# Performance work log

Measured on AMD Instinct MI355X. Metric: run time of the kernel, lower is better.

Reference implementation:

```python
import jax, jax.numpy as jnp
import numpy as np

TAU = 2.0
BN_EPS = 1e-5
SG_ALPHA = 4.0
ATTN_SCALE = 0.125
NUM_HEADS = 8
T, B, C, H, W = 2, 16, 256, 64, 64


@jax.custom_vjp
def heaviside(x):
    return (x >= 0.0).astype(x.dtype)

def _hv_fwd(x):
    return (x >= 0.0).astype(x.dtype), x

def _hv_bwd(x, g):
    s = jax.nn.sigmoid(SG_ALPHA * x)
    return (g * SG_ALPHA * s * (1.0 - s),)

heaviside.defvjp(_hv_fwd, _hv_bwd)


def lif(x_seq, v_th):
    # MultiStepLIFNode: v <- v + (x - v)/tau ; spike = H(v - v_th); hard reset to 0 (detached)
    def step(v, x):
        v = v + (x - v) / TAU
        s = heaviside(v - v_th)
        v = v * (1.0 - jax.lax.stop_gradient(s))
        return v, s
    _, spikes = jax.lax.scan(step, jnp.zeros_like(x_seq[0]), x_seq)
    return spikes


def bn1d(x, gamma, beta, mean, var):
    # eval-mode BatchNorm1d over channel axis 2 of [T,B,C,N]
    inv = (gamma / jnp.sqrt(var + BN_EPS)).reshape(1, 1, -1, 1)
    shift = (beta - mean * gamma / jnp.sqrt(var + BN_EPS)).reshape(1, 1, -1, 1)
    return x * inv + shift


def to_heads(t):
    # [T,B,C,N] -> [T,B,h,N,d]
    t_, b_, c_, n_ = t.shape
    d = c_ // NUM_HEADS
    return t.transpose(0, 1, 3, 2).reshape(t_, b_, n_, NUM_HEADS, d).transpose(0, 1, 3, 2, 4)


def setup_inputs() -> dict:
    key = jax.random.key(0)
    ks = jax.random.split(key, 24)
    w_scale = 0.06  # ~1/sqrt(C)
    inp = {
        'x': jax.random.normal(ks[0], (T, B, C, H, W), jnp.float32),
        'wq': jax.random.normal(ks[1], (C, C), jnp.float32) * w_scale,
        'wk': jax.random.normal(ks[2], (C, C), jnp.float32) * w_scale,
        'wv': jax.random.normal(ks[3], (C, C), jnp.float32) * w_scale,
        'wp': jax.random.normal(ks[4], (C, C), jnp.float32) * w_scale,
        'bp': jax.random.normal(ks[5], (C,), jnp.float32) * 0.1,
    }
    i = 6
    for p in ('q', 'k', 'v', 'p'):
        inp[p + '_gamma'] = jax.random.uniform(ks[i], (C,), jnp.float32, 0.5, 1.5); i += 1
        inp[p + '_beta'] = jax.random.normal(ks[i], (C,), jnp.float32) * 0.1; i += 1
        inp[p + '_mean'] = jax.random.normal(ks[i], (C,), jnp.float32) * 0.1; i += 1
        inp[p + '_var'] = jax.random.uniform(ks[i], (C,), jnp.float32, 0.5, 1.5); i += 1
    return inp


def reference(x, wq, wk, wv, wp, bp,
              q_gamma, q_beta, q_mean, q_var,
              k_gamma, k_beta, k_mean, k_var,
              v_gamma, v_beta, v_mean, v_var,
              p_gamma, p_beta, p_mean, p_var):
    t_, b_, c_, h_, w_ = x.shape
    n_ = h_ * w_
    xs = lif(x, 1.0).reshape(t_, b_, c_, n_)  # proj_lif then flatten(3)
    # 1x1 conv == channel matmul, then BN, then LIF (binary spikes)
    q_out = lif(bn1d(jnp.einsum('oc,tbcn->tbon', wq, xs), q_gamma, q_beta, q_mean, q_var), 1.0)
    k_out = lif(bn1d(jnp.einsum('oc,tbcn->tbon', wk, xs), k_gamma, k_beta, k_mean, k_var), 1.0)
    v_out = lif(bn1d(jnp.einsum('oc,tbcn->tbon', wv, xs), v_gamma, v_beta, v_mean, v_var), 1.0)
    q = to_heads(q_out)
    k = to_heads(k_out)
    v = to_heads(v_out)
    # linear attention: (k^T @ v) then q @ (k^T v)
    kv = jnp.einsum('tbhnd,tbhne->tbhde', k, v)  # [T,B,h,d,d]
    attn = jnp.einsum('tbhnd,tbhde->tbhne', q, kv) * ATTN_SCALE
    attn = attn.transpose(0, 1, 2, 4, 3).reshape(t_, b_, c_, n_)
    s = lif(attn, 0.5)  # attn_lif with v_threshold=0.5
    out = jnp.einsum('oc,tbcn->tbon', wp, s) + bp.reshape(1, 1, -1, 1)
    out = bn1d(out, p_gamma, p_beta, p_mean, p_var).reshape(t_, b_, c_, h_, w_)
    return (out, xs, q_out, k_out, v_out)
```

## Files before the change

kernel.cpp:

```cpp
#include <hip/hip_runtime.h>
#include <cstdint>
#include <cstddef>

typedef __attribute__((ext_vector_type(8))) short short8;
typedef __attribute__((ext_vector_type(4))) float floatx4;
typedef __attribute__((ext_vector_type(4))) unsigned int uintx4;
typedef __attribute__((ext_vector_type(4))) unsigned short ushort4x;

#define DEV static __device__ __forceinline__

constexpr int NT = 2, NB = 16, NC = 256, NN = 4096, NHD = 8;
constexpr size_t NE1 = (size_t)NT * NB * NC * NN;
constexpr size_t TSTRIDE = (size_t)NB * NC * NN;

DEV unsigned short f2bf(float x) {
  unsigned int u = __builtin_bit_cast(unsigned int, x);
  unsigned int lsb = (u >> 16) & 1u;
  u += 0x7FFFu + lsb;
  return (unsigned short)(u >> 16);
}
DEV float bfb2f(unsigned short h) {
  unsigned int u = ((unsigned int)h) << 16;
  return __builtin_bit_cast(float, u);
}
DEV unsigned short spike2bf(float s) {
  return (unsigned short)(__builtin_bit_cast(unsigned int, s) >> 16);
}
DEV unsigned int pk2(unsigned short a, unsigned short b) {
  return (unsigned int)a | ((unsigned int)b << 16);
}
DEV int swz(int fr, int kk) { return fr * 4 + (kk ^ ((fr >> 1) & 3)); }
typedef __attribute__((address_space(3))) unsigned int lds_u32;
typedef __attribute__((address_space(1))) const unsigned int glb_u32;
DEV void gld_lds16(const void* g, void* l) {
  __builtin_amdgcn_global_load_lds((glb_u32*)g, (lds_u32*)l, 16, 0, 0);
}

__global__ __launch_bounds__(256) void prep_kernel(
    const float* __restrict__ wq, const float* __restrict__ wk, const float* __restrict__ wv,
    const float* __restrict__ wp, const float* __restrict__ bp,
    const float* __restrict__ qg, const float* __restrict__ qb, const float* __restrict__ qm, const float* __restrict__ qva,
    const float* __restrict__ kg, const float* __restrict__ kb, const float* __restrict__ km, const float* __restrict__ kva,
    const float* __restrict__ vg, const float* __restrict__ vb, const float* __restrict__ vm, const float* __restrict__ vva,
    const float* __restrict__ pg, const float* __restrict__ pb, const float* __restrict__ pm, const float* __restrict__ pva,
    unsigned short* __restrict__ Wqkv, unsigned short* __restrict__ Wp,
    float* __restrict__ invqkv, float* __restrict__ shqkv,
    float* __restrict__ invp, float* __restrict__ shp)
{
  int idx = blockIdx.x * 256 + threadIdx.x;
  if (idx < 196608) {
    int o = idx >> 8, c = idx & 255;
    const float* src = (o < 256) ? wq : (o < 512) ? wk : wv;
    float w = src[(size_t)(o & 255) * 256 + c];
    unsigned short h0 = f2bf(w);  float f0 = bfb2f(h0);
    float r1 = w - f0;
    unsigned short h1 = f2bf(r1); float f1 = bfb2f(h1);
    float r2 = r1 - f1;
    unsigned short h2 = f2bf(r2);
    Wqkv[idx] = h0; Wqkv[196608 + idx] = h1; Wqkv[393216 + idx] = h2;
  } else if (idx < 262144) {
    int j = idx - 196608;
    float w = wp[j];
    unsigned short h0 = f2bf(w);  float f0 = bfb2f(h0);
    float r1 = w - f0;
    unsigned short h1 = f2bf(r1); float f1 = bfb2f(h1);
    float r2 = r1 - f1;
    unsigned short h2 = f2bf(r2);
    Wp[j] = h0; Wp[65536 + j] = h1; Wp[131072 + j] = h2;
  } else if (idx < 262912) {
    int i = idx - 262144;
    int p = i >> 8, c = i & 255;
    float g  = (p == 0) ? qg[c] : (p == 1) ? kg[c] : vg[c];
    float be = (p == 0) ? qb[c] : (p == 1) ? kb[c] : vb[c];
    float mn = (p == 0) ? qm[c] : (p == 1) ? km[c] : vm[c];
    float vr = (p == 0) ? qva[c] : (p == 1) ? kva[c] : vva[c];
    float sq = sqrtf(vr + 1e-5f);
    invqkv[i] = g / sq;
    shqkv[i]  = be - (mn * g) / sq;
  } else if (idx < 263168) {
    int c = idx - 262912;
    float sq = sqrtf(pva[c] + 1e-5f);
    float iv = pg[c] / sq;
    invp[c] = iv;
    shp[c]  = pb[c] - (pm[c] * pg[c]) / sq + bp[c] * iv;
  }
}

__global__ __launch_bounds__(256) void lifx_kernel(const float* __restrict__ x,
                                                   float* __restrict__ xs_out,
                                                   unsigned short* __restrict__ xs_t)
{
  __shared__ float tile[2][64][65];
  const int nt = blockIdx.x, ct = blockIdx.y, b = blockIdx.z;
  const int tid = threadIdx.x;
  const int ci = tid >> 2, cq = tid & 3;
  const int n0 = nt * 64, c0 = ct * 64;
  const size_t rowbase = ((size_t)(b * NC + c0 + ci)) * NN + n0 + cq * 16;
  const float* px0 = x + rowbase;
  const float* px1 = x + rowbase + TSTRIDE;
  float* po0 = xs_out + rowbase;
  float* po1 = xs_out + rowbase + TSTRIDE;
  #pragma unroll
  for (int jj = 0; jj < 4; jj++) {
    floatx4 x0 = *(const floatx4*)(px0 + jj * 4);
    floatx4 x1 = *(const floatx4*)(px1 + jj * 4);
    floatx4 s0v, s1v;
    #pragma unroll
    for (int e = 0; e < 4; e++) {
      float v1 = x0[e] * 0.5f;
      float s0 = (v1 >= 1.0f) ? 1.0f : 0.0f;
      float vr = v1 * (1.0f - s0);
      float v2 = vr + (x1[e] - vr) * 0.5f;
      float s1 = (v2 >= 1.0f) ? 1.0f : 0.0f;
      s0v[e] = s0; s1v[e] = s1;
      tile[0][ci][cq * 16 + jj * 4 + e] = s0;
      tile[1][ci][cq * 16 + jj * 4 + e] = s1;
    }
    *(floatx4*)(po0 + jj * 4) = s0v;
    *(floatx4*)(po1 + jj * 4) = s1v;
  }
  __syncthreads();
  const int ni = tid >> 2, cg = tid & 3;
  #pragma unroll
  for (int t = 0; t < 2; t++) {
    unsigned short* dst = xs_t + ((size_t)((t * NB + b) * NN) + n0 + ni) * NC + c0 + cg * 16;
    uintx4 w0, w1;
    #pragma unroll
    for (int p2 = 0; p2 < 4; p2++) {
      w0[p2] = pk2(spike2bf(tile[t][cg * 16 + p2 * 2    ][ni]),
                   spike2bf(tile[t][cg * 16 + p2 * 2 + 1][ni]));
      w1[p2] = pk2(spike2bf(tile[t][cg * 16 + p2 * 2 + 8][ni]),
                   spike2bf(tile[t][cg * 16 + p2 * 2 + 9][ni]));
    }
    *(uintx4*)dst = w0;
    *(uintx4*)(dst + 8) = w1;
  }
}

__global__ __launch_bounds__(256, 3) void qkv_gemm(
    const unsigned short* __restrict__ xs_t,
    const unsigned short* __restrict__ Wsp,
    const float* __restrict__ invv, const float* __restrict__ shv,
    float* __restrict__ dq, float* __restrict__ dk, float* __restrict__ dv,
    unsigned short* __restrict__ qbits, unsigned short* __restrict__ kbits,
    unsigned short* __restrict__ vbits)
{
  __shared__ __align__(16) unsigned char smem[33280];
  unsigned short* Al = (unsigned short*)smem;
  unsigned short* Bl = (unsigned short*)(smem + 24576);
  float* yl = (float*)smem;
  const int nt = blockIdx.x, mt = blockIdx.y, b = blockIdx.z;
  const int tid = threadIdx.x;
  const int lane = tid & 63, quad = lane >> 4, l16 = lane & 15;
  const int wave = tid >> 6;
  const int tw = wave >> 1, wm = (wave & 1) * 64;
  floatx4 acc[4][4] = {};

  for (int k0 = 0; k0 < 256; k0 += 32) {
    __syncthreads();
    #pragma unroll
    for (int j = 0; j < 6; j++) {
      int ci = j * 256 + tid;
      int fr = ci >> 2;
      int kk = (ci & 3) ^ ((fr >> 1) & 3);
      int s = fr >> 7, row = fr & 127;
      const unsigned short* g = Wsp + (size_t)s * 196608 + (size_t)(mt * 128 + row) * 256 + k0 + kk * 8;
      gld_lds16(g, Al + (size_t)ci * 8);
    }
    #pragma unroll
    for (int j = 0; j < 2; j++) {
      int ci = j * 256 + tid;
      int fr = ci >> 2;
      int kk = (ci & 3) ^ ((fr >> 1) & 3);
      int t = fr >> 6, row = fr & 63;
      const unsigned short* g = xs_t + ((size_t)((t * NB + b) * NN) + nt * 64 + row) * NC + k0 + kk * 8;
      gld_lds16(g, Bl + (size_t)ci * 8);
    }
    __syncthreads();

    short8 bfr[4];
    #pragma unroll
    for (int ni = 0; ni < 4; ni++) {
      int fr = tw * 64 + ni * 16 + l16;
      bfr[ni] = *(const short8*)(Bl + (size_t)swz(fr, quad) * 8);
    }
    #pragma unroll
    for (int mi = 0; mi < 4; mi++) {
      const int r0 = wm + mi * 16 + l16;
      short8 a0 = *(const short8*)(Al + (size_t)swz(      r0, quad) * 8);
      short8 a1 = *(const short8*)(Al + (size_t)swz(128 + r0, quad) * 8);
      short8 a2 = *(const short8*)(Al + (size_t)swz(256 + r0, quad) * 8);
      #pragma unroll
      for (int ni = 0; ni < 4; ni++) {
        acc[mi][ni] = __builtin_amdgcn_mfma_f32_16x16x32_bf16(a0, bfr[ni], acc[mi][ni], 0, 0, 0);
        acc[mi][ni] = __builtin_amdgcn_mfma_f32_16x16x32_bf16(a1, bfr[ni], acc[mi][ni], 0, 0, 0);
        acc[mi][ni] = __builtin_amdgcn_mfma_f32_16x16x32_bf16(a2, bfr[ni], acc[mi][ni], 0, 0, 0);
      }
    }
  }
  __syncthreads();
  if (tw == 0) {
    #pragma unroll
    for (int mi = 0; mi < 4; mi++)
      #pragma unroll
      for (int r = 0; r < 4; r++)
        #pragma unroll
        for (int ni = 0; ni < 4; ni++)
          yl[(size_t)(wm + mi * 16 + quad * 4 + r) * 65 + ni * 16 + l16] = acc[mi][ni][r];
  }
  __syncthreads();
  if (tw == 1) {
    #pragma unroll
    for (int mi = 0; mi < 4; mi++) {
      #pragma unroll
      for (int r = 0; r < 4; r++) {
        const int lrow = wm + mi * 16 + quad * 4 + r;
        const int orow = mt * 128 + lrow;
        const float iv = invv[orow], sh = shv[orow];
        const int widx = orow >> 8, c = orow & 255;
        float* dst = (widx == 0) ? dq : (widx == 1) ? dk : dv;
        unsigned short* bb = (widx == 0) ? qbits : (widx == 1) ? kbits : vbits;
        #pragma unroll
        for (int ni = 0; ni < 4; ni++) {
          const int n = nt * 64 + ni * 16 + l16;
          float y0 = yl[(size_t)lrow * 65 + ni * 16 + l16] * iv + sh;
          float y1 = acc[mi][ni][r] * iv + sh;
          float v1 = y0 * 0.5f;
          float s0 = (v1 >= 1.0f) ? 1.0f : 0.0f;
          float vr = v1 * (1.0f - s0);
          float v2 = vr + (y1 - vr) * 0.5f;
          float s1 = (v2 >= 1.0f) ? 1.0f : 0.0f;
          dst[(size_t)(b * NC + c) * NN + n] = s0;
          dst[(size_t)((NB + b) * NC + c) * NN + n] = s1;
          unsigned long long bl0 = __ballot(s0 != 0.0f);
          unsigned long long bl1 = __ballot(s1 != 0.0f);
          if (l16 == 0) {
            const int w16 = nt * 4 + ni;
            bb[(size_t)b        * 65536 + (size_t)c * 256 + w16] = (unsigned short)(bl0 >> (quad * 16));
            bb[(size_t)(NB + b) * 65536 + (size_t)c * 256 + w16] = (unsigned short)(bl1 >> (quad * 16));
          }
        }
      }
    }
  }
}

__global__ __launch_bounds__(256) void kv_kernel(const unsigned long long* __restrict__ kb,
                                                 const unsigned long long* __restrict__ vb,
                                                 float* __restrict__ kvout)
{
  __shared__ unsigned long long Kl[32 * 65];
  __shared__ unsigned long long Vl[32 * 65];
  const int h = blockIdx.x, z = blockIdx.y;
  const int tid = threadIdx.x;
  for (int i = tid; i < 2048; i += 256) {
    int row = i >> 6, w = i & 63;
    size_t g = (size_t)z * 16384 + (size_t)(h * 32 + row) * 64 + w;
    Kl[row * 65 + w] = kb[g];
    Vl[row * 65 + w] = vb[g];
  }
  __syncthreads();
  const int d = tid & 31, e0 = tid >> 5;
  int acc0 = 0, acc1 = 0, acc2 = 0, acc3 = 0;
  for (int w = 0; w < 64; w++) {
    unsigned long long ku = Kl[d * 65 + w];
    acc0 += __popcll(ku & Vl[(e0     ) * 65 + w]);
    acc1 += __popcll(ku & Vl[(e0 +  8) * 65 + w]);
    acc2 += __popcll(ku & Vl[(e0 + 16) * 65 + w]);
    acc3 += __popcll(ku & Vl[(e0 + 24) * 65 + w]);
  }
  float* o = kvout + ((size_t)(z * NHD + h) << 10);
  o[d * 32 + e0     ] = (float)acc0;
  o[d * 32 + e0 +  8] = (float)acc1;
  o[d * 32 + e0 + 16] = (float)acc2;
  o[d * 32 + e0 + 24] = (float)acc3;
}

__global__ __launch_bounds__(256) void attn_kernel(const unsigned short* __restrict__ qb16,
                                                   const float* __restrict__ kvout,
                                                   unsigned short* __restrict__ sb16)
{
  __shared__ float kvl[2][32][33];
  __shared__ unsigned short qt[2][32][16];
  const int nb = blockIdx.x, h = blockIdx.y, b = blockIdx.z;
  const int tid = threadIdx.x;
  const int wave = tid >> 6, lane = tid & 63, quad = lane >> 4, l16 = lane & 15;
  for (int i = tid; i < 2048; i += 256) {
    int t = i >> 10, j = i & 1023;
    kvl[t][j >> 5][j & 31] = kvout[((size_t)((t * NB + b) * NHD + h) << 10) + j];
  }
  for (int i = tid; i < 1024; i += 256) {
    int t = i >> 9, j = i & 511, row = j >> 4, w = j & 15;
    qt[t][row][w] = qb16[(size_t)(t * NB + b) * 65536 + (size_t)(h * 32 + row) * 256 + nb * 16 + w];
  }
  __syncthreads();
  short8 bf[2][2][2];
  #pragma unroll
  for (int t = 0; t < 2; t++) {
    #pragma unroll
    for (int eh = 0; eh < 2; eh++) {
      short8 bh, bl;
      #pragma unroll
      for (int j = 0; j < 8; j++) {
        float v = kvl[t][quad * 8 + j][eh * 16 + l16];
        unsigned short h0 = f2bf(v);
        float lo = v - bfb2f(h0);
        bh[j] = (short)h0;
        bl[j] = (short)f2bf(lo);
      }
      bf[t][0][eh] = bh; bf[t][1][eh] = bl;
    }
  }
  floatx4 acc[2][4][2] = {};
  #pragma unroll
  for (int t = 0; t < 2; t++) {
    #pragma unroll
    for (int nt = 0; nt < 4; nt++) {
      const int wv = wave * 4 + nt;
      short8 af;
      #pragma unroll
      for (int j = 0; j < 8; j++) {
        unsigned short w = qt[t][quad * 8 + j][wv];
        af[j] = (short)(((w >> l16) & 1) ? 0x3F80 : 0);
      }
      #pragma unroll
      for (int eh = 0; eh < 2; eh++) {
        acc[t][nt][eh] = __builtin_amdgcn_mfma_f32_16x16x32_bf16(af, bf[t][0][eh], acc[t][nt][eh], 0, 0, 0);
        acc[t][nt][eh] = __builtin_amdgcn_mfma_f32_16x16x32_bf16(af, bf[t][1][eh], acc[t][nt][eh], 0, 0, 0);
      }
    }
  }
  const int n0 = nb * 256 + wave * 64;
  #pragma unroll
  for (int nt = 0; nt < 4; nt++) {
    #pragma unroll
    for (int r = 0; r < 4; r++) {
      const int n = n0 + nt * 16 + quad * 4 + r;
      #pragma unroll
      for (int eh = 0; eh < 2; eh++) {
        float a0 = acc[0][nt][eh][r] * 0.125f;
        float a1 = acc[1][nt][eh][r] * 0.125f;
        float v1 = a0 * 0.5f;
        float s0 = (v1 >= 0.5f) ? 1.f : 0.f;
        float vr = v1 * (1.f - s0);
        float v2 = vr + (a1 - vr) * 0.5f;
        float s1 = (v2 >= 0.5f) ? 1.f : 0.f;
        unsigned long long bl0 = __ballot(s0 != 0.f);
        unsigned long long bl1 = __ballot(s1 != 0.f);
        if (l16 == 0) {
          const int w16 = h * 2 + eh;
          sb16[(size_t)b        * 65536 + (size_t)n * 16 + w16] = (unsigned short)(bl0 >> (quad * 16));
          sb16[(size_t)(NB + b) * 65536 + (size_t)n * 16 + w16] = (unsigned short)(bl1 >> (quad * 16));
        }
      }
    }
  }
}

__global__ __launch_bounds__(256, 3) void p_gemm(
    const unsigned short* __restrict__ sb16,
    const unsigned short* __restrict__ Wsp,
    const float* __restrict__ invv, const float* __restrict__ shv,
    float* __restrict__ dout)
{
  __shared__ __align__(16) unsigned char smem[32768];
  unsigned short* Al = (unsigned short*)smem;
  unsigned short* Bl = (unsigned short*)(smem + 24576);
  const int nt = blockIdx.x, mt = blockIdx.y, z = blockIdx.z;
  const int tid = threadIdx.x;
  const int lane = tid & 63, quad = lane >> 4, l16 = lane & 15;
  const int wave = tid >> 6;
  const int wm = (wave & 1) * 64, wn = (wave >> 1) * 64;
  floatx4 acc[4][4] = {};
  const int brow = tid & 127, bhalf = tid >> 7;

  for (int k0 = 0; k0 < 256; k0 += 32) {
    __syncthreads();
    #pragma unroll
    for (int j = 0; j < 6; j++) {
      int ci = j * 256 + tid;
      int fr = ci >> 2;
      int kk = (ci & 3) ^ ((fr >> 1) & 3);
      int s = fr >> 7, row = fr & 127;
      const unsigned short* g = Wsp + (size_t)s * 65536 + (size_t)(mt * 128 + row) * 256 + k0 + kk * 8;
      gld_lds16(g, Al + (size_t)ci * 8);
    }
    {
      unsigned short wb = sb16[(size_t)z * 65536 + (size_t)(nt * 128 + brow) * 16 + (k0 >> 4) + bhalf];
      uintx4 lo4, hi4;
      #pragma unroll
      for (int p = 0; p < 4; p++) {
        lo4[p] = pk2(((wb >> (2 * p)) & 1) ? 0x3F80 : 0, ((wb >> (2 * p + 1)) & 1) ? 0x3F80 : 0);
        hi4[p] = pk2(((wb >> (8 + 2 * p)) & 1) ? 0x3F80 : 0, ((wb >> (9 + 2 * p)) & 1) ? 0x3F80 : 0);
      }
      *(uintx4*)(Bl + (size_t)swz(brow, bhalf * 2)     * 8) = lo4;
      *(uintx4*)(Bl + (size_t)swz(brow, bhalf * 2 + 1) * 8) = hi4;
    }
    __syncthreads();

    short8 bfr[4];
    #pragma unroll
    for (int ni = 0; ni < 4; ni++) {
      int fr = wn + ni * 16 + l16;
      bfr[ni] = *(const short8*)(Bl + (size_t)swz(fr, quad) * 8);
    }
    #pragma unroll
    for (int mi = 0; mi < 4; mi++) {
      const int r0 = wm + mi * 16 + l16;
      short8 a0 = *(const short8*)(Al + (size_t)swz(      r0, quad) * 8);
      short8 a1 = *(const short8*)(Al + (size_t)swz(128 + r0, quad) * 8);
      short8 a2 = *(const short8*)(Al + (size_t)swz(256 + r0, quad) * 8);
      #pragma unroll
      for (int ni = 0; ni < 4; ni++) {
        acc[mi][ni] = __builtin_amdgcn_mfma_f32_16x16x32_bf16(a0, bfr[ni], acc[mi][ni], 0, 0, 0);
        acc[mi][ni] = __builtin_amdgcn_mfma_f32_16x16x32_bf16(a1, bfr[ni], acc[mi][ni], 0, 0, 0);
        acc[mi][ni] = __builtin_amdgcn_mfma_f32_16x16x32_bf16(a2, bfr[ni], acc[mi][ni], 0, 0, 0);
      }
    }
  }
  #pragma unroll
  for (int mi = 0; mi < 4; mi++) {
    #pragma unroll
    for (int r = 0; r < 4; r++) {
      const int orow = mt * 128 + wm + mi * 16 + quad * 4 + r;
      const float iv = invv[orow], sh = shv[orow];
      #pragma unroll
      for (int ni = 0; ni < 4; ni++) {
        const int n = nt * 128 + wn + ni * 16 + l16;
        dout[((size_t)(z * NC + orow)) * NN + n] = acc[mi][ni][r] * iv + sh;
      }
    }
  }
}

extern "C" void kernel_launch(void* const* d_in, const int* in_sizes, int n_in,
                              void* d_out, int out_size, void* d_ws, size_t ws_size,
                              hipStream_t stream) {
  (void)in_sizes; (void)n_in; (void)out_size; (void)ws_size;
  const float* x  = (const float*)d_in[0];
  const float* wq = (const float*)d_in[1];
  const float* wk = (const float*)d_in[2];
  const float* wv = (const float*)d_in[3];
  const float* wp = (const float*)d_in[4];
  const float* bp = (const float*)d_in[5];
  const float* qg = (const float*)d_in[6],  *qb = (const float*)d_in[7];
  const float* qm = (const float*)d_in[8],  *qva = (const float*)d_in[9];
  const float* kg = (const float*)d_in[10], *kb = (const float*)d_in[11];
  const float* km = (const float*)d_in[12], *kva = (const float*)d_in[13];
  const float* vg = (const float*)d_in[14], *vb = (const float*)d_in[15];
  const float* vm = (const float*)d_in[16], *vva = (const float*)d_in[17];
  const float* pg = (const float*)d_in[18], *pb = (const float*)d_in[19];
  const float* pm = (const float*)d_in[20], *pva = (const float*)d_in[21];

  float* out = (float*)d_out;
  float* xs  = out + NE1;
  float* dq  = out + 2 * NE1;
  float* dk  = out + 3 * NE1;
  float* dv  = out + 4 * NE1;

  char* ws = (char*)d_ws;
  unsigned short* xs_t  = (unsigned short*)ws;
  unsigned short* Wqkv  = (unsigned short*)(ws + 67108864);
  unsigned short* Wp    = (unsigned short*)(ws + 68288512);
  float* kvout          = (float*)(ws + 68681728);
  unsigned short* qbits = (unsigned short*)(ws + 69730304);
  unsigned short* kbits = (unsigned short*)(ws + 73924608);
  unsigned short* vbits = (unsigned short*)(ws + 78118912);
  unsigned short* sbits = (unsigned short*)(ws + 82313216);
  float* invqkv         = (float*)(ws + 86507520);
  float* shqkv          = invqkv + 768;
  float* invp           = shqkv + 768;
  float* shp            = invp + 256;

  prep_kernel<<<1028, 256, 0, stream>>>(wq, wk, wv, wp, bp,
                                        qg, qb, qm, qva, kg, kb, km, kva,
                                        vg, vb, vm, vva, pg, pb, pm, pva,
                                        Wqkv, Wp, invqkv, shqkv, invp, shp);
  lifx_kernel<<<dim3(64, 4, 16), 256, 0, stream>>>(x, xs, xs_t);
  qkv_gemm<<<dim3(64, 6, 16), 256, 0, stream>>>(xs_t, Wqkv, invqkv, shqkv,
                                                dq, dk, dv, qbits, kbits, vbits);
  kv_kernel<<<dim3(8, 32), 256, 0, stream>>>((const unsigned long long*)kbits,
                                             (const unsigned long long*)vbits, kvout);
  attn_kernel<<<dim3(16, 8, 16), 256, 0, stream>>>(qbits, kvout, sbits);
  p_gemm<<<dim3(32, 2, 32), 256, 0, stream>>>(sbits, Wp, invp, shp, out);
}
```

Before: 1.035 ms.

## Store input spikes as packed bitmasks and expand to bf16 in GEMM

The LIF input kernel now writes the spike tensor as 16-bit bitmasks per 16 channels instead of a transposed bf16 copy, shrinking that intermediate sixteen-fold. The QKV GEMM reads the bitmask words and expands them into bf16 ones and zeros in registers before writing the swizzled LDS tile, replacing the async global-to-LDS loads for the B operand. This cuts global write and read traffic for the intermediate. It adds ALU work and synchronous LDS stores inside the GEMM loop, and issues small 2-byte global loads.

```diff
diff --git a/kernel.cpp b/kernel.cpp
--- a/kernel.cpp
+++ b/kernel.cpp
@@ -5,7 +5,6 @@
 typedef __attribute__((ext_vector_type(8))) short short8;
 typedef __attribute__((ext_vector_type(4))) float floatx4;
 typedef __attribute__((ext_vector_type(4))) unsigned int uintx4;
-typedef __attribute__((ext_vector_type(4))) unsigned short ushort4x;
 
 #define DEV static __device__ __forceinline__
 
@@ -22,9 +21,6 @@
 DEV float bfb2f(unsigned short h) {
   unsigned int u = ((unsigned int)h) << 16;
   return __builtin_bit_cast(float, u);
-}
-DEV unsigned short spike2bf(float s) {
-  return (unsigned short)(__builtin_bit_cast(unsigned int, s) >> 16);
 }
 DEV unsigned int pk2(unsigned short a, unsigned short b) {
   return (unsigned int)a | ((unsigned int)b << 16);
@@ -88,7 +84,7 @@
 
 __global__ __launch_bounds__(256) void lifx_kernel(const float* __restrict__ x,
                                                    float* __restrict__ xs_out,
-                                                   unsigned short* __restrict__ xs_t)
+                                                   unsigned short* __restrict__ xb16)
 {
   __shared__ float tile[2][64][65];
   const int nt = blockIdx.x, ct = blockIdx.y, b = blockIdx.z;
@@ -123,22 +119,16 @@
   const int ni = tid >> 2, cg = tid & 3;
   #pragma unroll
   for (int t = 0; t < 2; t++) {
-    unsigned short* dst = xs_t + ((size_t)((t * NB + b) * NN) + n0 + ni) * NC + c0 + cg * 16;
-    uintx4 w0, w1;
-    #pragma unroll
-    for (int p2 = 0; p2 < 4; p2++) {
-      w0[p2] = pk2(spike2bf(tile[t][cg * 16 + p2 * 2    ][ni]),
-                   spike2bf(tile[t][cg * 16 + p2 * 2 + 1][ni]));
-      w1[p2] = pk2(spike2bf(tile[t][cg * 16 + p2 * 2 + 8][ni]),
-                   spike2bf(tile[t][cg * 16 + p2 * 2 + 9][ni]));
-    }
-    *(uintx4*)dst = w0;
-    *(uintx4*)(dst + 8) = w1;
+    unsigned int wbits = 0;
+    #pragma unroll
+    for (int j = 0; j < 16; j++)
+      wbits |= (tile[t][cg * 16 + j][ni] != 0.f ? 1u : 0u) << j;
+    xb16[((size_t)((t * NB + b) * NN) + n0 + ni) * 16 + (c0 >> 4) + cg] = (unsigned short)wbits;
   }
 }
 
 __global__ __launch_bounds__(256, 3) void qkv_gemm(
-    const unsigned short* __restrict__ xs_t,
+    const unsigned short* __restrict__ xb16,
     const unsigned short* __restrict__ Wsp,
     const float* __restrict__ invv, const float* __restrict__ shv,
     float* __restrict__ dq, float* __restrict__ dk, float* __restrict__ dv,
@@ -155,6 +145,8 @@
   const int wave = tid >> 6;
   const int tw = wave >> 1, wm = (wave & 1) * 64;
   floatx4 acc[4][4] = {};
+  const int bt = tid >> 7, brow = (tid >> 1) & 63, bhalf = tid & 1;
+  const unsigned short* xrow = xb16 + ((size_t)((bt * NB + b) * NN) + nt * 64 + brow) * 16 + bhalf;
 
   for (int k0 = 0; k0 < 256; k0 += 32) {
     __syncthreads();
@@ -167,14 +159,17 @@
       const unsigned short* g = Wsp + (size_t)s * 196608 + (size_t)(mt * 128 + row) * 256 + k0 + kk * 8;
       gld_lds16(g, Al + (size_t)ci * 8);
     }
-    #pragma unroll
-    for (int j = 0; j < 2; j++) {
-      int ci = j * 256 + tid;
-      int fr = ci >> 2;
-      int kk = (ci & 3) ^ ((fr >> 1) & 3);
-      int t = fr >> 6, row = fr & 63;
-      const unsigned short* g = xs_t + ((size_t)((t * NB + b) * NN) + nt * 64 + row) * NC + k0 + kk * 8;
-      gld_lds16(g, Bl + (size_t)ci * 8);
+    {
+      unsigned int wb = xrow[k0 >> 4];
+      uintx4 c0v, c1v;
+      #pragma unroll
+      for (int p = 0; p < 4; p++) {
+        c0v[p] = pk2(((wb >> (2 * p)) & 1) ? 0x3F80 : 0, ((wb >> (2 * p + 1)) & 1) ? 0x3F80 : 0);
+        c1v[p] = pk2(((wb >> (8 + 2 * p)) & 1) ? 0x3F80 : 0, ((wb >> (9 + 2 * p)) & 1) ? 0x3F80 : 0);
+      }
+      int fr = bt * 64 + brow;
+      *(uintx4*)(Bl + (size_t)swz(fr, bhalf * 2)     * 8) = c0v;
+      *(uintx4*)(Bl + (size_t)swz(fr, bhalf * 2 + 1) * 8) = c1v;
     }
     __syncthreads();
 
@@ -459,15 +454,15 @@
   float* dv  = out + 4 * NE1;
 
   char* ws = (char*)d_ws;
-  unsigned short* xs_t  = (unsigned short*)ws;
-  unsigned short* Wqkv  = (unsigned short*)(ws + 67108864);
-  unsigned short* Wp    = (unsigned short*)(ws + 68288512);
-  float* kvout          = (float*)(ws + 68681728);
-  unsigned short* qbits = (unsigned short*)(ws + 69730304);
-  unsigned short* kbits = (unsigned short*)(ws + 73924608);
-  unsigned short* vbits = (unsigned short*)(ws + 78118912);
-  unsigned short* sbits = (unsigned short*)(ws + 82313216);
-  float* invqkv         = (float*)(ws + 86507520);
+  unsigned short* xbits = (unsigned short*)ws;
+  unsigned short* Wqkv  = (unsigned short*)(ws + 4194304);
+  unsigned short* Wp    = (unsigned short*)(ws + 5373952);
+  float* kvout          = (float*)(ws + 5767168);
+  unsigned short* qbits = (unsigned short*)(ws + 6815744);
+  unsigned short* kbits = (unsigned short*)(ws + 11010048);
+  unsigned short* vbits = (unsigned short*)(ws + 15204352);
+  unsigned short* sbits = (unsigned short*)(ws + 19398656);
+  float* invqkv         = (float*)(ws + 23592960);
   float* shqkv          = invqkv + 768;
   float* invp           = shqkv + 768;
   float* shp            = invp + 256;
@@ -476,8 +471,8 @@
                                         qg, qb, qm, qva, kg, kb, km, kva,
                                         vg, vb, vm, vva, pg, pb, pm, pva,
                                         Wqkv, Wp, invqkv, shqkv, invp, shp);
-  lifx_kernel<<<dim3(64, 4, 16), 256, 0, stream>>>(x, xs, xs_t);
-  qkv_gemm<<<dim3(64, 6, 16), 256, 0, stream>>>(xs_t, Wqkv, invqkv, shqkv,
+  lifx_kernel<<<dim3(64, 4, 16), 256, 0, stream>>>(x, xs, xbits);
+  qkv_gemm<<<dim3(64, 6, 16), 256, 0, stream>>>(xbits, Wqkv, invqkv, shqkv,
                                                 dq, dk, dv, qbits, kbits, vbits);
   kv_kernel<<<dim3(8, 32), 256, 0, stream>>>((const unsigned long long*)kbits,
                                              (const unsigned long long*)vbits, kvout);
```

Result: faster. 974.5 us (-5.9%).
